# Kernel optimization log

Hardware: AMD Instinct MI355X
Metric: run time of the kernel (lower is better)

Reference implementation:

```python
import jax, jax.numpy as jnp
import numpy as np

NB_LAYERS, KSIZE = 4, 5
DILATIONS = [1, 2, 4, 8]
NEG_SLOPE = 0.1
BN_EPS = 1e-5


def _cont_conv(times, feats, mask, dilation, p):
    """One ContConv1d layer: causal gather of time-diffs -> kernel MLP -> weighted aggregate + skip + BN."""
    k1W, k1b, k2W, k2b, k3W, k3b, skipW, skipb, gamma, beta = p
    bs, L, Cin = feats.shape
    Cout = skipW.shape[1]
    lags = jnp.arange(KSIZE) * dilation                    # (K,) include_zero_lag=True -> lag 0 included
    idx = jnp.arange(L)[None, :] - lags[:, None]           # (K, L) causal neighbor indices
    valid = idx >= 0
    idx_c = jnp.clip(idx, 0, L - 1)
    g_times = times[:, idx_c]                              # (bs, K, L)
    g_feats = feats[:, idx_c, :]                           # (bs, K, L, Cin)
    g_mask = (mask[:, idx_c] & valid[None] & mask[:, None, :]).astype(feats.dtype)
    dt = (times[:, None, :] - g_times) * g_mask            # (bs, K, L) zeroed where invalid
    # kernel MLP: scalar time-diff -> (Cin, Cout) mixing matrix
    h = jax.nn.leaky_relu(dt[..., None] @ k1W + k1b, NEG_SLOPE)
    h = jax.nn.leaky_relu(h @ k2W + k2b, NEG_SLOPE)
    kv = (h @ k3W + k3b).reshape(bs, KSIZE, L, Cin, Cout) * g_mask[..., None, None]
    out = jnp.einsum('bklc,bklcd->bld', g_feats, kv)       # aggregate over taps and input channels
    out = out + feats @ skipW + skipb                      # 1x1-conv skip connection
    mu = out.mean((0, 1))                                  # BatchNorm1d (training-mode batch stats)
    var = out.var((0, 1))
    return (out - mu) * jax.lax.rsqrt(var + BN_EPS) * gamma + beta


def _ccnn_forward(event_times, event_types, emb, k1W, k1b, k2W, k2b, k3W, k3b, skipW, skipb, gamma, beta):
    bs = event_times.shape[0]
    emb = emb.at[0].set(0.0)                               # padding_idx = 0
    times = jnp.concatenate([jnp.zeros((bs, 1), event_times.dtype), event_times], axis=1)
    bos = jnp.full((bs, 1), jnp.max(event_types) + 1, dtype=event_types.dtype)
    types = jnp.concatenate([bos, event_types], axis=1)
    mask = times != 0                                      # BOS (t=0) masked, as in the original
    enc = emb[types]                                       # (bs, L+1, C)
    for i in range(NB_LAYERS):
        p = (k1W[i], k1b[i], k2W[i], k2b[i], k3W[i], k3b[i], skipW[i], skipb[i], gamma[i], beta[i])
        enc = jax.nn.leaky_relu(_cont_conv(times, enc, mask, DILATIONS[i], p), NEG_SLOPE)
    return enc


def setup_inputs() -> dict:
    key = jax.random.key(0)
    ks = jax.random.split(key, 12)
    bs, L, C, H, num_types = 8, 2048, 32, 16, 100
    s = 0.05
    gaps = jax.random.uniform(ks[0], (bs, L)) * 0.1 + 0.01
    times = jnp.cumsum(gaps, axis=1)                       # strictly increasing positive event times
    types = jax.random.randint(ks[1], (bs, L), 0, num_types) + 1   # 1..num_types
    pad = jnp.arange(L) >= int(0.9 * L)
    times = jnp.where(pad[None, :], 0.0, times).astype(jnp.float32)
    types = jnp.where(pad[None, :], 0, types).astype(jnp.int32)
    return {
        'event_times': times,
        'event_types': types,
        'emb': jax.random.normal(ks[2], (num_types + 2, C)) * s,
        'k1W': jax.random.normal(ks[3], (NB_LAYERS, 1, H)) * s,
        'k1b': jnp.zeros((NB_LAYERS, H)),
        'k2W': jax.random.normal(ks[4], (NB_LAYERS, H, H)) * s,
        'k2b': jnp.zeros((NB_LAYERS, H)),
        'k3W': jax.random.normal(ks[5], (NB_LAYERS, H, C * C)) * s,
        'k3b': jnp.zeros((NB_LAYERS, C * C)),
        'skipW': jax.random.normal(ks[6], (NB_LAYERS, C, C)) * s,
        'skipb': jnp.zeros((NB_LAYERS, C)),
        'gamma': jnp.ones((NB_LAYERS, C)),
        'beta': jnp.zeros((NB_LAYERS, C)),
    }


def reference(event_times, event_types, emb, k1W, k1b, k2W, k2b, k3W, k3b, skipW, skipb, gamma, beta):
    return _ccnn_forward(event_times, event_types, emb, k1W, k1b, k2W, k2b, k3W, k3b, skipW, skipb, gamma, beta)
```

## Files before the change

kernel.cpp:

```cpp
#include <hip/hip_runtime.h>
#include <stdint.h>

#define NB_LAYERS 4
#define KSIZE 5
#define BSZ 8
#define LIN 2048
#define LSEQ 2049
#define CCH 32
#define HCH 16
#define MROWS (BSZ*LSEQ)
#define NTILES ((MROWS+15)/16)
#define NEG 0.1f
#define BNEPS 1e-5f
#define CONVGRID 129
#define CONVBLK 512
#define NWAVES (CONVBLK/64)
#define NJOBS (NWAVES*KSIZE*16)
#define NFRAG 36
#define WT_HALVES (NFRAG*64*8)

typedef _Float16 h2v __attribute__((ext_vector_type(2)));
typedef _Float16 h8v __attribute__((ext_vector_type(8)));
typedef float    f4v __attribute__((ext_vector_type(4)));

union H8 { h8v v; h2v h[4]; };

static __device__ __forceinline__ h2v mkh2(float a, float b) {
  h2v r; r[0] = (_Float16)a; r[1] = (_Float16)b; return r;
}

static __device__ __forceinline__ void wt_decode(
    int g, const float* __restrict__ k3Wl, const float* __restrict__ k3bl,
    const float* __restrict__ skipWl, int& halfidx, float& val) {
  int n, k;
  if (g < 16384)      { n = g & 31; int c = (g >> 5) & 31; int h = g >> 10; k = h * 32 + c; val = k3Wl[g]; }
  else if (g < 17408) { int g2 = g - 16384; n = g2 & 31; int c = g2 >> 5; k = 512 + c; val = k3bl[g2]; }
  else                { int g2 = g - 17408; n = g2 & 31; int c = g2 >> 5; k = 544 + c; val = skipWl[g2]; }
  int m = n & 15, a = n >> 4, qq = (k >> 3) & 3, hh = k & 7;
  int f = (k < 512) ? ((k >> 5) * 2 + a) : ((k < 544) ? (32 + a) : (34 + a));
  halfidx = f * 512 + ((qq << 4) | m) * 8 + hh;
}

template<int MODE>
__global__ __launch_bounds__(CONVBLK) void conv_kernel(
    const float* __restrict__ enc_in,
    const int*   __restrict__ types,
    const float* __restrict__ emb,
    float* __restrict__ enc_out,
    const float* __restrict__ etimes,
    const float* __restrict__ k1Wp, const float* __restrict__ k1bp,
    const float* __restrict__ k2Wp, const float* __restrict__ k2bp,
    const float* __restrict__ k3W, const float* __restrict__ k3b,
    const float* __restrict__ skipW,
    _Float16* __restrict__ WtG,
    const float* __restrict__ stats_prev,
    const float* __restrict__ partials_prev,
    float* __restrict__ stats_out,
    float* __restrict__ partials_out,
    float* __restrict__ stats_zero,
    const float* __restrict__ gamma_prev, const float* __restrict__ beta_prev,
    int dil)
{
  __shared__ h8v Wl[(MODE == 1) ? (NFRAG * 64) : 1];
  __shared__ h8v swh[NWAVES * KSIZE * 16 * 2];
  __shared__ alignas(16) float sW[304];
  __shared__ float sst[64];
  __shared__ float sbn[64];

  const int tid  = threadIdx.x;
  const int lane = tid & 63;
  const int wv   = tid >> 6;
  const int m    = lane & 15;
  const int q    = lane >> 4;
  const int bid  = blockIdx.x;

  if (tid < 64) { sst[tid] = 0.f; sbn[tid] = 0.f; }
  if (tid < 16) { sW[tid] = k1Wp[tid]; sW[16 + tid] = k1bp[tid]; sW[32 + tid] = k2bp[tid]; }
  if (tid >= 64 && tid < 320) sW[48 + tid - 64] = k2Wp[tid - 64];

  if (MODE == 0) {
    if (bid == 0 && tid < 192) stats_zero[tid] = 0.f;
    int id2 = bid * CONVBLK + tid;
    if (id2 < 3 * WT_HALVES) {
      int layer = 1 + id2 / WT_HALVES;
      int g = id2 - (layer - 1) * WT_HALVES;
      int hi; float val;
      wt_decode(g, k3W + layer * 16384, k3b + layer * 1024, skipW + layer * 1024, hi, val);
      WtG[(layer - 1) * WT_HALVES + hi] = (_Float16)val;
    }
  } else {
    const float4* src = (const float4*)WtG;
    float4* dst = (float4*)Wl;
#pragma unroll
    for (int i = 0; i < 5; i++) {
      int idx = tid + i * CONVBLK;
      if (idx < WT_HALVES / 8) dst[idx] = src[idx];
    }
  }
  __syncthreads();

  if (MODE == 1 && partials_prev) {
    float v = 0.f;
#pragma unroll 4
    for (int i = tid; i < CONVGRID * 64; i += CONVBLK) v += partials_prev[i];
    atomicAdd(&sbn[tid & 63], v);
    __syncthreads();
  }

  float sc8[8], ob8[8];
  if (MODE == 1) {
    const float inv = 1.f / (float)MROWS;
#pragma unroll
    for (int j = 0; j < 8; j++) {
      int c = q * 8 + j;
      float s1 = partials_prev ? sbn[c]      : stats_prev[c];
      float s2 = partials_prev ? sbn[32 + c] : stats_prev[32 + c];
      float mu = s1 * inv;
      float var = s2 * inv - mu * mu;
      float sc = gamma_prev[c] * rsqrtf(var + BNEPS);
      sc8[j] = sc; ob8[j] = beta_prev[c] - mu * sc;
    }
  }

  const int tile = bid * NWAVES + wv;
  const bool deadtile = (tile >= NTILES);

  int row = tile * 16 + m;
  bool rvalid = row < MROWS;
  int rowc = min(row, MROWS - 1);
  int b = rowc / LSEQ, pos = rowc % LSEQ;
  float t_l = (pos == 0) ? 0.f : etimes[b * LIN + pos - 1];
  bool mask_l = rvalid && (t_l != 0.f);

  float4 fa[KSIZE], fbv[KSIZE];
  int tts[KSIZE];
  int jcs[KSIZE]; float tjv[KSIZE];
  if (!deadtile) {
    int bosv = 0;
    if (MODE == 0) {
      if (__ballot(pos == 0)) {
        const int4* tp = (const int4*)types;
        int mx = 0;
#pragma unroll 4
        for (int i = lane; i < (BSZ * LIN) / 4; i += 64) {
          int4 v = tp[i];
          mx = max(mx, max(max(v.x, v.y), max(v.z, v.w)));
        }
#pragma unroll
        for (int off = 32; off; off >>= 1) mx = max(mx, __shfl_xor(mx, off, 64));
        bosv = mx + 1;
      }
    }
#pragma unroll
    for (int tap = 0; tap < KSIZE; tap++) {
      int j = pos - tap * dil;
      int jc = max(j, 0); jcs[tap] = jc;
      tjv[tap] = (jc == 0) ? 0.f : etimes[b * LIN + jc - 1];
    }
    if (MODE == 0) {
#pragma unroll
      for (int tap = 0; tap < KSIZE; tap++) {
        int jc = jcs[tap];
        tts[tap] = (jc > 0) ? types[b * LIN + jc - 1] : ((tap == 0) ? bosv : 0);
      }
#pragma unroll
      for (int tap = 0; tap < KSIZE; tap++) {
        const float* ep = emb + tts[tap] * CCH + q * 8;
        fa[tap] = *(const float4*)ep; fbv[tap] = *(const float4*)(ep + 4);
      }
    } else {
#pragma unroll
      for (int tap = 0; tap < KSIZE; tap++) {
        const float* fp = enc_in + (b * LSEQ + jcs[tap]) * CCH + q * 8;
        fa[tap] = *(const float4*)fp; fbv[tap] = *(const float4*)(fp + 4);
      }
    }
  }

#pragma unroll
  for (int rep = 0; rep < 2; rep++) {
    const int job = rep ? (512 + tid) : tid;
    const bool act = rep ? (tid < 128) : true;
    const int jj2 = act ? job : 0;
    const int wvt = jj2 / 80;
    const int rr  = jj2 % 80;
    const int tap = rr / 16;
    const int jrow = rr % 16;
    const int tile_t = bid * NWAVES + wvt;
    int row_t = tile_t * 16 + jrow;
    bool rvalid_t = row_t < MROWS;
    int rowc_t = min(row_t, MROWS - 1);
    int b_t = rowc_t / LSEQ, pos_t = rowc_t % LSEQ;
    float tl_t = (pos_t == 0) ? 0.f : etimes[b_t * LIN + pos_t - 1];
    int j2 = pos_t - tap * dil;
    int jc2 = max(j2, 0);
    float tj2 = (jc2 == 0) ? 0.f : etimes[b_t * LIN + jc2 - 1];
    bool g2 = act && rvalid_t && (tl_t != 0.f) && (j2 >= 0) && (tj2 != 0.f);
    float dt = g2 ? (tl_t - tj2) : 0.f;

    H8 w0, w1;
    if (__ballot(g2)) {
      const f4v* k1wv = (const f4v*)&sW[0];
      const f4v* k1bv = (const f4v*)&sW[16];
      const f4v* k2bv = (const f4v*)&sW[32];
      float h1[HCH], h2[HCH];
#pragma unroll
      for (int h4 = 0; h4 < 4; h4++) {
        f4v cw = k1wv[h4], cb = k1bv[h4], c2 = k2bv[h4];
#pragma unroll
        for (int r = 0; r < 4; r++) {
          float x = fmaf(dt, cw[r], cb[r]);
          h1[h4*4+r] = fmaxf(x, NEG * x);
          h2[h4*4+r] = c2[r];
        }
      }
#pragma unroll
      for (int hp = 0; hp < HCH; hp++) {
        float hv = h1[hp];
        const f4v* kk = (const f4v*)&sW[48 + hp * 16];
#pragma unroll
        for (int h4 = 0; h4 < 4; h4++) {
          f4v c = kk[h4];
#pragma unroll
          for (int r = 0; r < 4; r++) h2[h4*4+r] = fmaf(hv, c[r], h2[h4*4+r]);
        }
      }
      float g = g2 ? 1.f : 0.f;
#pragma unroll
      for (int p2 = 0; p2 < 4; p2++) {
        float a0 = h2[2*p2];     a0 = fmaxf(a0, NEG * a0) * g;
        float a1 = h2[2*p2+1];   a1 = fmaxf(a1, NEG * a1) * g;
        w0.h[p2] = mkh2(a0, a1);
        float b0 = h2[8+2*p2];   b0 = fmaxf(b0, NEG * b0) * g;
        float b1 = h2[8+2*p2+1]; b1 = fmaxf(b1, NEG * b1) * g;
        w1.h[p2] = mkh2(b0, b1);
      }
    } else {
#pragma unroll
      for (int p2 = 0; p2 < 4; p2++) { w0.h[p2] = mkh2(0.f, 0.f); w1.h[p2] = mkh2(0.f, 0.f); }
    }
    if (act) {
      int base = ((wvt * KSIZE + tap) * 16 + jrow) * 2;
      swh[base] = w0.v; swh[base + 1] = w1.v;
    }
  }

  h2v fh[KSIZE][4];
  h2v fself[4];
  float Fb[8];
  if (!deadtile) {
#pragma unroll
    for (int jj = 0; jj < 8; jj++) Fb[jj] = 0.f;
#pragma unroll
    for (int tap = 0; tap < KSIZE; tap++) {
      bool gm = mask_l && (pos - tap * dil >= 0) && (tjv[tap] != 0.f);
      float fv[8] = {fa[tap].x, fa[tap].y, fa[tap].z, fa[tap].w,
                     fbv[tap].x, fbv[tap].y, fbv[tap].z, fbv[tap].w};
      if (MODE == 0) {
        float zf = (tts[tap] != 0) ? 1.f : 0.f;
#pragma unroll
        for (int jj = 0; jj < 8; jj++) fv[jj] *= zf;
      } else {
#pragma unroll
        for (int jj = 0; jj < 8; jj++) {
          float x = fmaf(fv[jj], sc8[jj], ob8[jj]);
          fv[jj] = fmaxf(x, NEG * x);
        }
      }
      if (tap == 0) {
        float rv = rvalid ? 1.f : 0.f;
#pragma unroll
        for (int p2 = 0; p2 < 4; p2++) fself[p2] = mkh2(fv[2*p2] * rv, fv[2*p2+1] * rv);
      }
      float g = gm ? 1.f : 0.f;
#pragma unroll
      for (int jj = 0; jj < 8; jj++) Fb[jj] += g * fv[jj];
#pragma unroll
      for (int p2 = 0; p2 < 4; p2++) fh[tap][p2] = mkh2(fv[2*p2], fv[2*p2+1]);
    }
  }
  __syncthreads();

  if (!deadtile) {
    h2v wh[KSIZE][8];
#pragma unroll
    for (int tap = 0; tap < KSIZE; tap++) {
      int base = ((wv * KSIZE + tap) * 16 + m) * 2;
      H8 a0, a1; a0.v = swh[base]; a1.v = swh[base + 1];
#pragma unroll
      for (int p2 = 0; p2 < 4; p2++) { wh[tap][p2] = a0.h[p2]; wh[tap][4+p2] = a1.h[p2]; }
    }

    f4v aP = {0,0,0,0}, aQ = {0,0,0,0}, bP = {0,0,0,0}, bQ = {0,0,0,0};

#pragma unroll
    for (int ks = 0; ks < 16; ks++) {
      H8 bf0, bf1, af;
      if (MODE == 0) {
        const float* wp = k3W + ks * 1024 + (q * 8) * 32 + m;
#pragma unroll
        for (int p2 = 0; p2 < 4; p2++) {
          bf0.h[p2] = mkh2(wp[(2*p2) * 32],      wp[(2*p2+1) * 32]);
          bf1.h[p2] = mkh2(wp[(2*p2) * 32 + 16], wp[(2*p2+1) * 32 + 16]);
        }
      } else {
        bf0.v = Wl[(2*ks + 0) * 64 + lane];
        bf1.v = Wl[(2*ks + 1) * 64 + lane];
      }
      h2v u0 = mkh2(0.f,0.f), u1 = mkh2(0.f,0.f), u2 = mkh2(0.f,0.f), u3 = mkh2(0.f,0.f);
#pragma unroll
      for (int tap = 0; tap < KSIZE; tap++) {
        _Float16 w = wh[tap][ks >> 1][ks & 1];
        h2v wd; wd[0] = w; wd[1] = w;
        u0 += wd * fh[tap][0];
        u1 += wd * fh[tap][1];
        u2 += wd * fh[tap][2];
        u3 += wd * fh[tap][3];
      }
      af.h[0] = u0; af.h[1] = u1; af.h[2] = u2; af.h[3] = u3;
      if (ks & 1) {
        aQ = __builtin_amdgcn_mfma_f32_16x16x32_f16(af.v, bf0.v, aQ, 0, 0, 0);
        bQ = __builtin_amdgcn_mfma_f32_16x16x32_f16(af.v, bf1.v, bQ, 0, 0, 0);
      } else {
        aP = __builtin_amdgcn_mfma_f32_16x16x32_f16(af.v, bf0.v, aP, 0, 0, 0);
        bP = __builtin_amdgcn_mfma_f32_16x16x32_f16(af.v, bf1.v, bP, 0, 0, 0);
      }
    }
    {
      H8 bf0, bf1, af;
      if (MODE == 0) {
        const float* kp = k3b + (q * 8) * 32 + m;
#pragma unroll
        for (int p2 = 0; p2 < 4; p2++) {
          bf0.h[p2] = mkh2(kp[(2*p2) * 32],      kp[(2*p2+1) * 32]);
          bf1.h[p2] = mkh2(kp[(2*p2) * 32 + 16], kp[(2*p2+1) * 32 + 16]);
        }
      } else {
        bf0.v = Wl[32 * 64 + lane];
        bf1.v = Wl[33 * 64 + lane];
      }
#pragma unroll
      for (int p2 = 0; p2 < 4; p2++) af.h[p2] = mkh2(Fb[2*p2], Fb[2*p2+1]);
      aP = __builtin_amdgcn_mfma_f32_16x16x32_f16(af.v, bf0.v, aP, 0, 0, 0);
      bP = __builtin_amdgcn_mfma_f32_16x16x32_f16(af.v, bf1.v, bP, 0, 0, 0);
    }
    {
      H8 bf0, bf1, af;
      if (MODE == 0) {
        const float* sp = skipW + (q * 8) * 32 + m;
#pragma unroll
        for (int p2 = 0; p2 < 4; p2++) {
          bf0.h[p2] = mkh2(sp[(2*p2) * 32],      sp[(2*p2+1) * 32]);
          bf1.h[p2] = mkh2(sp[(2*p2) * 32 + 16], sp[(2*p2+1) * 32 + 16]);
        }
      } else {
        bf0.v = Wl[34 * 64 + lane];
        bf1.v = Wl[35 * 64 + lane];
      }
      af.h[0] = fself[0]; af.h[1] = fself[1]; af.h[2] = fself[2]; af.h[3] = fself[3];
      aQ = __builtin_amdgcn_mfma_f32_16x16x32_f16(af.v, bf0.v, aQ, 0, 0, 0);
      bQ = __builtin_amdgcn_mfma_f32_16x16x32_f16(af.v, bf1.v, bQ, 0, 0, 0);
    }
    f4v acc0 = aP + aQ;
    f4v acc1 = bP + bQ;

    float s0 = 0.f, s1 = 0.f, s2 = 0.f, s3 = 0.f;
#pragma unroll
    for (int r = 0; r < 4; r++) {
      float v0 = acc0[r], v1 = acc1[r];
      s0 += v0; s1 += v0 * v0; s2 += v1; s3 += v1 * v1;
      int rd = tile * 16 + q * 4 + r;
      if (rd < MROWS) {
        enc_out[rd * CCH + m] = v0;
        enc_out[rd * CCH + 16 + m] = v1;
      }
    }
    s0 += __shfl_xor(s0, 16, 64); s0 += __shfl_xor(s0, 32, 64);
    s1 += __shfl_xor(s1, 16, 64); s1 += __shfl_xor(s1, 32, 64);
    s2 += __shfl_xor(s2, 16, 64); s2 += __shfl_xor(s2, 32, 64);
    s3 += __shfl_xor(s3, 16, 64); s3 += __shfl_xor(s3, 32, 64);
    if (q == 0) {
      atomicAdd(&sst[m], s0);
      atomicAdd(&sst[32 + m], s1);
      atomicAdd(&sst[16 + m], s2);
      atomicAdd(&sst[48 + m], s3);
    }
  }
  __syncthreads();
  if (tid < 64) {
    if (MODE == 0) partials_out[bid * 64 + tid] = sst[tid];
    else           atomicAdd(&stats_out[tid], sst[tid]);
  }
}

__global__ __launch_bounds__(256) void bn_kernel(
    const float* __restrict__ x, float* __restrict__ out,
    const float* __restrict__ stats,
    const float* __restrict__ gamma, const float* __restrict__ beta) {
  int idx0 = blockIdx.x * 256 + threadIdx.x;
  int c0 = (idx0 * 4) & 31;
  const float inv = 1.f / (float)MROWS;
  float sc[4], ob[4];
#pragma unroll
  for (int r = 0; r < 4; r++) {
    int c = c0 + r;
    float mu = stats[c] * inv;
    float var = stats[32 + c] * inv - mu * mu;
    sc[r] = gamma[c] * rsqrtf(var + BNEPS);
    ob[r] = beta[c] - mu * sc[r];
  }
  for (int i = idx0; i < (MROWS * CCH) / 4; i += 256 * 256) {
    float4 v = ((const float4*)x)[i];
    float4 o;
    o.x = fmaf(v.x, sc[0], ob[0]); o.x = fmaxf(o.x, NEG * o.x);
    o.y = fmaf(v.y, sc[1], ob[1]); o.y = fmaxf(o.y, NEG * o.y);
    o.z = fmaf(v.z, sc[2], ob[2]); o.z = fmaxf(o.z, NEG * o.z);
    o.w = fmaf(v.w, sc[3], ob[3]); o.w = fmaxf(o.w, NEG * o.w);
    ((float4*)out)[i] = o;
  }
}

extern "C" void kernel_launch(void* const* d_in, const int* in_sizes, int n_in,
                              void* d_out, int out_size, void* d_ws, size_t ws_size,
                              hipStream_t stream) {
  (void)in_sizes; (void)n_in; (void)out_size; (void)ws_size;
  const float* event_times = (const float*)d_in[0];
  const int*   event_types = (const int*)d_in[1];
  const float* emb   = (const float*)d_in[2];
  const float* k1W   = (const float*)d_in[3];
  const float* k1b   = (const float*)d_in[4];
  const float* k2W   = (const float*)d_in[5];
  const float* k2b   = (const float*)d_in[6];
  const float* k3W   = (const float*)d_in[7];
  const float* k3b   = (const float*)d_in[8];
  const float* skipW = (const float*)d_in[9];
  const float* gamma = (const float*)d_in[11];
  const float* beta  = (const float*)d_in[12];

  float* enc_a = (float*)d_ws;
  float* enc_b = enc_a + (size_t)MROWS * CCH;
  float* stats = enc_b + (size_t)MROWS * CCH;
  float* partials0 = stats + NB_LAYERS * 64;
  _Float16* Wt = (_Float16*)(((uintptr_t)(partials0 + CONVGRID * 64) + 255) & ~(uintptr_t)255);

  conv_kernel<0><<<CONVGRID, CONVBLK, 0, stream>>>(
      nullptr, event_types, emb, enc_b, event_times,
      k1W, k1b, k2W, k2b, k3W, k3b, skipW, Wt,
      nullptr, nullptr, nullptr, partials0, stats + 64,
      nullptr, nullptr, 1);

  conv_kernel<1><<<CONVGRID, CONVBLK, 0, stream>>>(
      enc_b, nullptr, nullptr, enc_a, event_times,
      k1W + HCH, k1b + HCH, k2W + HCH*HCH, k2b + HCH,
      nullptr, nullptr, nullptr, Wt + 0 * WT_HALVES,
      nullptr, partials0, stats + 64, nullptr, nullptr,
      gamma + 0 * CCH, beta + 0 * CCH, 2);

  conv_kernel<1><<<CONVGRID, CONVBLK, 0, stream>>>(
      enc_a, nullptr, nullptr, enc_b, event_times,
      k1W + 2*HCH, k1b + 2*HCH, k2W + 2*HCH*HCH, k2b + 2*HCH,
      nullptr, nullptr, nullptr, Wt + 1 * WT_HALVES,
      stats + 64, nullptr, stats + 128, nullptr, nullptr,
      gamma + 1 * CCH, beta + 1 * CCH, 4);

  conv_kernel<1><<<CONVGRID, CONVBLK, 0, stream>>>(
      enc_b, nullptr, nullptr, enc_a, event_times,
      k1W + 3*HCH, k1b + 3*HCH, k2W + 3*HCH*HCH, k2b + 3*HCH,
      nullptr, nullptr, nullptr, Wt + 2 * WT_HALVES,
      stats + 128, nullptr, stats + 192, nullptr, nullptr,
      gamma + 2 * CCH, beta + 2 * CCH, 8);

  bn_kernel<<<256, 256, 0, stream>>>(enc_a, (float*)d_out,
      stats + 192, gamma + 3 * CCH, beta + 3 * CCH);
}
```

Before: 143.9 us.

## Split each tile's K-reduction across two waves and combine via shared memory

Each 16-row tile is now handled by a pair of waves. Each wave processes half the kernel-MLP K slices (even or odd), and one of them also takes the bias or skip MFMA. Partial accumulators are combined through a new shared buffer after a barrier, so the grid doubles to keep every row covered. This halves the serial MFMA chain per wave and raises wave-level parallelism, at the cost of an extra __syncthreads, more LDS traffic, duplicated per-tile gathers and activation work in both waves, and twice the per-block weight staging.

```diff
diff --git a/kernel.cpp b/kernel.cpp
--- a/kernel.cpp
+++ b/kernel.cpp
@@ -12,10 +12,10 @@
 #define NTILES ((MROWS+15)/16)
 #define NEG 0.1f
 #define BNEPS 1e-5f
-#define CONVGRID 129
+#define CONVGRID 257
 #define CONVBLK 512
-#define NWAVES (CONVBLK/64)
-#define NJOBS (NWAVES*KSIZE*16)
+#define NTILEPB 4
+#define NJOBS (NTILEPB*KSIZE*16)
 #define NFRAG 36
 #define WT_HALVES (NFRAG*64*8)
 
@@ -62,7 +62,8 @@
     int dil)
 {
   __shared__ h8v Wl[(MODE == 1) ? (NFRAG * 64) : 1];
-  __shared__ h8v swh[NWAVES * KSIZE * 16 * 2];
+  __shared__ h8v swh[NTILEPB * KSIZE * 16 * 2];
+  __shared__ float cmb[NTILEPB][64][9];
   __shared__ alignas(16) float sW[304];
   __shared__ float sst[64];
   __shared__ float sbn[64];
@@ -73,6 +74,8 @@
   const int m    = lane & 15;
   const int q    = lane >> 4;
   const int bid  = blockIdx.x;
+  const int role   = wv & 1;
+  const int tilein = wv >> 1;
 
   if (tid < 64) { sst[tid] = 0.f; sbn[tid] = 0.f; }
   if (tid < 16) { sW[tid] = k1Wp[tid]; sW[16 + tid] = k1bp[tid]; sW[32 + tid] = k2bp[tid]; }
@@ -122,7 +125,7 @@
     }
   }
 
-  const int tile = bid * NWAVES + wv;
+  const int tile = bid * NTILEPB + tilein;
   const bool deadtile = (tile >= NTILES);
 
   int row = tile * 16 + m;
@@ -177,16 +180,14 @@
     }
   }
 
-#pragma unroll
-  for (int rep = 0; rep < 2; rep++) {
-    const int job = rep ? (512 + tid) : tid;
-    const bool act = rep ? (tid < 128) : true;
-    const int jj2 = act ? job : 0;
-    const int wvt = jj2 / 80;
-    const int rr  = jj2 % 80;
+  {
+    const bool act = tid < NJOBS;
+    const int job = act ? tid : 0;
+    const int tilein_t = job / 80;
+    const int rr  = job % 80;
     const int tap = rr / 16;
     const int jrow = rr % 16;
-    const int tile_t = bid * NWAVES + wvt;
+    const int tile_t = bid * NTILEPB + tilein_t;
     int row_t = tile_t * 16 + jrow;
     bool rvalid_t = row_t < MROWS;
     int rowc_t = min(row_t, MROWS - 1);
@@ -240,7 +241,7 @@
       for (int p2 = 0; p2 < 4; p2++) { w0.h[p2] = mkh2(0.f, 0.f); w1.h[p2] = mkh2(0.f, 0.f); }
     }
     if (act) {
-      int base = ((wvt * KSIZE + tap) * 16 + jrow) * 2;
+      int base = ((tilein_t * KSIZE + tap) * 16 + jrow) * 2;
       swh[base] = w0.v; swh[base + 1] = w1.v;
     }
   }
@@ -281,20 +282,20 @@
   }
   __syncthreads();
 
+  f4v accA = {0,0,0,0}, accB = {0,0,0,0};
   if (!deadtile) {
     h2v wh[KSIZE][8];
 #pragma unroll
     for (int tap = 0; tap < KSIZE; tap++) {
-      int base = ((wv * KSIZE + tap) * 16 + m) * 2;
+      int base = ((tilein * KSIZE + tap) * 16 + m) * 2;
       H8 a0, a1; a0.v = swh[base]; a1.v = swh[base + 1];
 #pragma unroll
       for (int p2 = 0; p2 < 4; p2++) { wh[tap][p2] = a0.h[p2]; wh[tap][4+p2] = a1.h[p2]; }
     }
 
-    f4v aP = {0,0,0,0}, aQ = {0,0,0,0}, bP = {0,0,0,0}, bQ = {0,0,0,0};
-
-#pragma unroll
-    for (int ks = 0; ks < 16; ks++) {
+#pragma unroll
+    for (int i = 0; i < 8; i++) {
+      const int ks = 2 * i + role;
       H8 bf0, bf1, af;
       if (MODE == 0) {
         const float* wp = k3W + ks * 1024 + (q * 8) * 32 + m;
@@ -310,7 +311,7 @@
       h2v u0 = mkh2(0.f,0.f), u1 = mkh2(0.f,0.f), u2 = mkh2(0.f,0.f), u3 = mkh2(0.f,0.f);
 #pragma unroll
       for (int tap = 0; tap < KSIZE; tap++) {
-        _Float16 w = wh[tap][ks >> 1][ks & 1];
+        _Float16 w = role ? wh[tap][i][1] : wh[tap][i][0];
         h2v wd; wd[0] = w; wd[1] = w;
         u0 += wd * fh[tap][0];
         u1 += wd * fh[tap][1];
@@ -318,51 +319,50 @@
         u3 += wd * fh[tap][3];
       }
       af.h[0] = u0; af.h[1] = u1; af.h[2] = u2; af.h[3] = u3;
-      if (ks & 1) {
-        aQ = __builtin_amdgcn_mfma_f32_16x16x32_f16(af.v, bf0.v, aQ, 0, 0, 0);
-        bQ = __builtin_amdgcn_mfma_f32_16x16x32_f16(af.v, bf1.v, bQ, 0, 0, 0);
-      } else {
-        aP = __builtin_amdgcn_mfma_f32_16x16x32_f16(af.v, bf0.v, aP, 0, 0, 0);
-        bP = __builtin_amdgcn_mfma_f32_16x16x32_f16(af.v, bf1.v, bP, 0, 0, 0);
-      }
+      accA = __builtin_amdgcn_mfma_f32_16x16x32_f16(af.v, bf0.v, accA, 0, 0, 0);
+      accB = __builtin_amdgcn_mfma_f32_16x16x32_f16(af.v, bf1.v, accB, 0, 0, 0);
     }
     {
       H8 bf0, bf1, af;
       if (MODE == 0) {
-        const float* kp = k3b + (q * 8) * 32 + m;
+        const float* tp2 = role ? (skipW + (q * 8) * 32 + m) : (k3b + (q * 8) * 32 + m);
 #pragma unroll
         for (int p2 = 0; p2 < 4; p2++) {
-          bf0.h[p2] = mkh2(kp[(2*p2) * 32],      kp[(2*p2+1) * 32]);
-          bf1.h[p2] = mkh2(kp[(2*p2) * 32 + 16], kp[(2*p2+1) * 32 + 16]);
+          bf0.h[p2] = mkh2(tp2[(2*p2) * 32],      tp2[(2*p2+1) * 32]);
+          bf1.h[p2] = mkh2(tp2[(2*p2) * 32 + 16], tp2[(2*p2+1) * 32 + 16]);
         }
       } else {
-        bf0.v = Wl[32 * 64 + lane];
-        bf1.v = Wl[33 * 64 + lane];
-      }
-#pragma unroll
-      for (int p2 = 0; p2 < 4; p2++) af.h[p2] = mkh2(Fb[2*p2], Fb[2*p2+1]);
-      aP = __builtin_amdgcn_mfma_f32_16x16x32_f16(af.v, bf0.v, aP, 0, 0, 0);
-      bP = __builtin_amdgcn_mfma_f32_16x16x32_f16(af.v, bf1.v, bP, 0, 0, 0);
-    }
-    {
-      H8 bf0, bf1, af;
-      if (MODE == 0) {
-        const float* sp = skipW + (q * 8) * 32 + m;
-#pragma unroll
-        for (int p2 = 0; p2 < 4; p2++) {
-          bf0.h[p2] = mkh2(sp[(2*p2) * 32],      sp[(2*p2+1) * 32]);
-          bf1.h[p2] = mkh2(sp[(2*p2) * 32 + 16], sp[(2*p2+1) * 32 + 16]);
-        }
+        int f0 = role ? 34 : 32;
+        bf0.v = Wl[f0 * 64 + lane];
+        bf1.v = Wl[(f0 + 1) * 64 + lane];
+      }
+      if (role == 0) {
+#pragma unroll
+        for (int p2 = 0; p2 < 4; p2++) af.h[p2] = mkh2(Fb[2*p2], Fb[2*p2+1]);
       } else {
-        bf0.v = Wl[34 * 64 + lane];
-        bf1.v = Wl[35 * 64 + lane];
-      }
-      af.h[0] = fself[0]; af.h[1] = fself[1]; af.h[2] = fself[2]; af.h[3] = fself[3];
-      aQ = __builtin_amdgcn_mfma_f32_16x16x32_f16(af.v, bf0.v, aQ, 0, 0, 0);
-      bQ = __builtin_amdgcn_mfma_f32_16x16x32_f16(af.v, bf1.v, bQ, 0, 0, 0);
-    }
-    f4v acc0 = aP + aQ;
-    f4v acc1 = bP + bQ;
+        af.h[0] = fself[0]; af.h[1] = fself[1]; af.h[2] = fself[2]; af.h[3] = fself[3];
+      }
+      accA = __builtin_amdgcn_mfma_f32_16x16x32_f16(af.v, bf0.v, accA, 0, 0, 0);
+      accB = __builtin_amdgcn_mfma_f32_16x16x32_f16(af.v, bf1.v, accB, 0, 0, 0);
+    }
+  }
+
+  if (!deadtile && role == 1) {
+#pragma unroll
+    for (int r = 0; r < 4; r++) {
+      cmb[tilein][lane][r]     = accA[r];
+      cmb[tilein][lane][4 + r] = accB[r];
+    }
+  }
+  __syncthreads();
+
+  if (!deadtile && role == 0) {
+    f4v acc0, acc1;
+#pragma unroll
+    for (int r = 0; r < 4; r++) {
+      acc0[r] = accA[r] + cmb[tilein][lane][r];
+      acc1[r] = accB[r] + cmb[tilein][lane][4 + r];
+    }
 
     float s0 = 0.f, s1 = 0.f, s2 = 0.f, s3 = 0.f;
 #pragma unroll
```

After: 146.9 us. +2.0%, slower.
